# Kernel tuning notes

Hardware: AMD Instinct MI355X
Metric: run time of the kernel (lower is better)

## Reference

```python
import jax, jax.numpy as jnp
import numpy as np

DIM = 1024
N_HEADS = 16
HEAD_DIM = DIM // N_HEADS


def setup_inputs() -> dict:
    key = jax.random.key(0)
    ks = jax.random.split(key, 5)
    x = jax.random.normal(ks[0], (2, 2048, DIM), dtype=jnp.float32)
    # nn.Linear-style init scale
    s = 1.0 / np.sqrt(DIM)
    W_qkv = jax.random.uniform(ks[1], (DIM, 3 * DIM), jnp.float32, -s, s)
    b_qkv = jax.random.uniform(ks[2], (3 * DIM,), jnp.float32, -s, s)
    W_proj = jax.random.uniform(ks[3], (DIM, DIM), jnp.float32, -s, s)
    b_proj = jax.random.uniform(ks[4], (DIM,), jnp.float32, -s, s)
    return {"x": x, "W_qkv": W_qkv, "b_qkv": b_qkv, "W_proj": W_proj, "b_proj": b_proj}


def reference(x, W_qkv, b_qkv, W_proj, b_proj):
    B, S, D = x.shape
    scale = HEAD_DIM ** -0.5
    qkv = x @ W_qkv + b_qkv                                   # [B,S,3D]
    qkv = qkv.reshape(B, S, 3, N_HEADS, HEAD_DIM)
    q = qkv[:, :, 0].transpose(0, 2, 1, 3)                    # [B,H,S,d]
    k = qkv[:, :, 1].transpose(0, 2, 1, 3)
    v = qkv[:, :, 2].transpose(0, 2, 1, 3)
    attn = jnp.einsum('bhqd,bhkd->bhqk', q, k) * scale        # [B,H,S,S]
    attn = jax.nn.softmax(attn, axis=-1)
    out = jnp.einsum('bhqk,bhkd->bhqd', attn, v)              # [B,H,S,d]
    out = out.transpose(0, 2, 1, 3).reshape(B, S, D)
    return out @ W_proj + b_proj
```

## Files before the change

### kernel.cpp

```cpp
#include <hip/hip_runtime.h>
#include <stdint.h>

typedef unsigned short u16;
typedef __attribute__((ext_vector_type(8))) short bf16x8;
typedef __attribute__((ext_vector_type(4))) float f32x4;
typedef __attribute__((ext_vector_type(4))) u16 us4;
typedef __attribute__((ext_vector_type(8))) u16 us8;

__device__ __forceinline__ u16 f2bf(float f) {
  union { float f; unsigned u; } v; v.f = f;
  unsigned r = v.u + 0x7fffu + ((v.u >> 16) & 1u);
  return (u16)(r >> 16);
}

__device__ __forceinline__ void gld16(const void* g, void* l) {
  __builtin_amdgcn_global_load_lds(
      (const __attribute__((address_space(1))) void*)g,
      (__attribute__((address_space(3))) void*)l, 16, 0, 0);
}

__global__ void cvt_kernel(const float* __restrict__ in, u16* __restrict__ out, int n4) {
  int i = blockIdx.x * blockDim.x + threadIdx.x;
  if (i >= n4) return;
  f32x4 v = ((const f32x4*)in)[i];
  us4 r;
#pragma unroll
  for (int j = 0; j < 4; ++j) r[j] = f2bf(v[j]);
  ((us4*)out)[i] = r;
}

__global__ void transw_kernel(const float* __restrict__ in, u16* __restrict__ out, int R, int C) {
  __shared__ u16 tile[32][33];
  const int tx = threadIdx.x & 31, ty = threadIdx.x >> 5;
  const int c0 = blockIdx.x * 32, r0 = blockIdx.y * 32;
#pragma unroll
  for (int j = 0; j < 4; ++j)
    tile[ty + j * 8][tx] = f2bf(in[(size_t)(r0 + ty + j * 8) * C + c0 + tx]);
  __syncthreads();
#pragma unroll
  for (int j = 0; j < 4; ++j)
    out[(size_t)(c0 + ty + j * 8) * R + r0 + tx] = tile[tx][ty + j * 8];
}

__global__ __launch_bounds__(256) void qkv_gemm_kernel(
    const u16* __restrict__ A, const u16* __restrict__ Bt, const float* __restrict__ bias,
    u16* __restrict__ Qb, u16* __restrict__ Kb, u16* __restrict__ Vtb) {
  __shared__ u16 sm[17408];
  u16* As = sm;
  u16* Bs = sm + 4096;
  const int tid = threadIdx.x;
  const int w = tid >> 6, l = tid & 63, quad = l >> 4, lanelo = l & 15;
  const int wr = w >> 1, wc = w & 1;
  const long m0 = (long)blockIdx.x * 128;
  const long n0 = (long)blockIdx.y * 128;

  f32x4 acc[4][4];
#pragma unroll
  for (int i = 0; i < 4; ++i)
#pragma unroll
    for (int j = 0; j < 4; ++j) acc[i][j] = (f32x4){0.f, 0.f, 0.f, 0.f};

  const u16* ag = A + (m0 + w * 32 + (l >> 2)) * 1024 + (l & 3) * 8;
  const u16* bg = Bt + (n0 + w * 32 + (l >> 2)) * 1024 + (l & 3) * 8;
  u16* asl = As + w * 1024;
  u16* bsl = Bs + w * 1024;

  for (int kt = 0; kt < 32; ++kt) {
    const int ko = kt * 32;
    gld16(ag + ko, asl);
    gld16(ag + 16 * 1024 + ko, asl + 512);
    gld16(bg + ko, bsl);
    gld16(bg + 16 * 1024 + ko, bsl + 512);
    __syncthreads();
    bf16x8 af[4], bf[4];
#pragma unroll
    for (int mt = 0; mt < 4; ++mt)
      af[mt] = *(const bf16x8*)(As + (wr * 64 + mt * 16 + lanelo) * 32 + quad * 8);
#pragma unroll
    for (int nt = 0; nt < 4; ++nt)
      bf[nt] = *(const bf16x8*)(Bs + (wc * 64 + nt * 16 + lanelo) * 32 + quad * 8);
#pragma unroll
    for (int mt = 0; mt < 4; ++mt)
#pragma unroll
      for (int nt = 0; nt < 4; ++nt)
        acc[mt][nt] = __builtin_amdgcn_mfma_f32_16x16x32_bf16(af[mt], bf[nt], acc[mt][nt], 0, 0, 0);
    __syncthreads();
  }

  float bias_v[4];
#pragma unroll
  for (int nt = 0; nt < 4; ++nt) bias_v[nt] = bias[n0 + wc * 64 + nt * 16 + lanelo];

  u16* Ct = sm;
#pragma unroll
  for (int mt = 0; mt < 4; ++mt)
#pragma unroll
    for (int nt = 0; nt < 4; ++nt)
#pragma unroll
      for (int r = 0; r < 4; ++r)
        Ct[(wr * 64 + mt * 16 + quad * 4 + r) * 136 + wc * 64 + nt * 16 + lanelo] =
            f2bf(acc[mt][nt][r] + bias_v[nt]);
  __syncthreads();

  const int b = (int)(m0 >> 11);
  const int s0 = (int)(m0 & 2047);
  const int t = (int)(n0 >> 10);
  const int h0 = (int)((n0 & 1023) >> 6);

  if (t < 2) {
    u16* dst = (t == 0) ? Qb : Kb;
#pragma unroll
    for (int p = 0; p < 8; ++p) {
      const int hh = p >> 2;
      const int sl = (p & 3) * 32 + (tid >> 3);
      const int c8 = tid & 7;
      us8 v = *(const us8*)(Ct + sl * 136 + hh * 64 + c8 * 8);
      const int pos = (c8 + sl) & 7;
      const size_t off = ((size_t)((b * 16 + h0 + hh) * 2048 + s0 + sl)) * 64 + pos * 8;
      *(us8*)(dst + off) = v;
    }
  } else {
#pragma unroll
    for (int p = 0; p < 8; ++p) {
      const int hh = p >> 2;
      const int dl = (p & 3) * 16 + (tid >> 4);
      const int c16 = tid & 15;
      us8 v;
#pragma unroll
      for (int j = 0; j < 8; ++j) v[j] = Ct[(c16 * 8 + j) * 136 + hh * 64 + dl];
      const int pos = (c16 + dl) & 15;
      const size_t off = ((size_t)((b * 16 + h0 + hh) * 64 + dl)) * 2048 + s0 + pos * 8;
      *(us8*)(Vtb + off) = v;
    }
  }
}

__global__ __launch_bounds__(256) void attn_kernel(
    const u16* __restrict__ Qb, const u16* __restrict__ Kb,
    const u16* __restrict__ Vtb, u16* __restrict__ Ob) {
  __shared__ u16 Ks[128 * 64];
  __shared__ u16 Vs[64 * 128];
  __shared__ u16 Ps[4][32 * 128];
  const int tid = threadIdx.x;
  const int w = tid >> 6, l = tid & 63, quad = l >> 4, lanelo = l & 15;
  const int qt = blockIdx.x, head = blockIdx.y;
  const int b = head >> 4, h = head & 15;
  const u16* Qh = Qb + (size_t)head * 2048 * 64;
  const u16* Kh = Kb + (size_t)head * 2048 * 64;
  const u16* Vh = Vtb + (size_t)head * 64 * 2048;
  u16* Pw = &Ps[w][0];

  const float C = 0.18033688011112042f;

  bf16x8 qf[2][2];
#pragma unroll
  for (int mt = 0; mt < 2; ++mt)
#pragma unroll
    for (int ks = 0; ks < 2; ++ks) {
      const int row = qt * 128 + w * 32 + mt * 16 + lanelo;
      const int pos = (ks * 4 + quad + lanelo) & 7;
      qf[mt][ks] = *(const bf16x8*)(Qh + (size_t)row * 64 + pos * 8);
    }

  f32x4 o[2][4], os[2];
#pragma unroll
  for (int mt = 0; mt < 2; ++mt) {
    os[mt] = (f32x4){0.f, 0.f, 0.f, 0.f};
#pragma unroll
    for (int ot = 0; ot < 4; ++ot) o[mt][ot] = (f32x4){0.f, 0.f, 0.f, 0.f};
  }
  bf16x8 ones;
#pragma unroll
  for (int j = 0; j < 8; ++j) ones[j] = (short)0x3F80;

  for (int kt = 0; kt < 16; ++kt) {
    const u16* kbase = Kh + kt * 8192;
#pragma unroll
    for (int j = 0; j < 4; ++j) {
      const int i = w * 4 + j;
      gld16(kbase + i * 512 + l * 8, &Ks[i * 512]);
    }
#pragma unroll
    for (int j = 0; j < 4; ++j) {
      const int i = w * 4 + j;
      const int dd = i * 4 + (l >> 4);
      gld16(Vh + (size_t)dd * 2048 + kt * 128 + (l & 15) * 8, &Vs[i * 512]);
    }
    __syncthreads();

    f32x4 s[2][8];
#pragma unroll
    for (int mt = 0; mt < 2; ++mt)
#pragma unroll
      for (int nt = 0; nt < 8; ++nt) s[mt][nt] = (f32x4){0.f, 0.f, 0.f, 0.f};

#pragma unroll
    for (int ks = 0; ks < 2; ++ks) {
#pragma unroll
      for (int nt = 0; nt < 8; ++nt) {
        const int keyl = nt * 16 + lanelo;
        const int pos = (ks * 4 + quad + lanelo) & 7;
        bf16x8 kf = *(const bf16x8*)(&Ks[keyl * 64 + pos * 8]);
        s[0][nt] = __builtin_amdgcn_mfma_f32_16x16x32_bf16(qf[0][ks], kf, s[0][nt], 0, 0, 0);
        s[1][nt] = __builtin_amdgcn_mfma_f32_16x16x32_bf16(qf[1][ks], kf, s[1][nt], 0, 0, 0);
      }
    }

#pragma unroll
    for (int mt = 0; mt < 2; ++mt)
#pragma unroll
      for (int nt = 0; nt < 8; ++nt)
#pragma unroll
        for (int r = 0; r < 4; ++r) {
          const float p = exp2f(s[mt][nt][r] * C);
          const int row = mt * 16 + quad * 4 + r;
          const int pos = (2 * nt + (lanelo >> 3) + row) & 15;
          Pw[row * 128 + pos * 8 + (lanelo & 7)] = f2bf(p);
        }

#pragma unroll
    for (int ks = 0; ks < 4; ++ks) {
      bf16x8 pf[2];
#pragma unroll
      for (int mt = 0; mt < 2; ++mt) {
        const int row = mt * 16 + lanelo;
        const int pos = (ks * 4 + quad + lanelo) & 15;
        pf[mt] = *(const bf16x8*)(&Pw[row * 128 + pos * 8]);
      }
      os[0] = __builtin_amdgcn_mfma_f32_16x16x32_bf16(pf[0], ones, os[0], 0, 0, 0);
      os[1] = __builtin_amdgcn_mfma_f32_16x16x32_bf16(pf[1], ones, os[1], 0, 0, 0);
#pragma unroll
      for (int ot = 0; ot < 4; ++ot) {
        const int dim = ot * 16 + lanelo;
        const int pos = (ks * 4 + quad + lanelo) & 15;
        bf16x8 vf = *(const bf16x8*)(&Vs[dim * 128 + pos * 8]);
        o[0][ot] = __builtin_amdgcn_mfma_f32_16x16x32_bf16(pf[0], vf, o[0][ot], 0, 0, 0);
        o[1][ot] = __builtin_amdgcn_mfma_f32_16x16x32_bf16(pf[1], vf, o[1][ot], 0, 0, 0);
      }
    }
    __syncthreads();
  }

#pragma unroll
  for (int mt = 0; mt < 2; ++mt)
#pragma unroll
    for (int r = 0; r < 4; ++r) {
      const float inv = 1.0f / os[mt][r];
      const int srow = qt * 128 + w * 32 + mt * 16 + quad * 4 + r;
      const size_t base = ((size_t)(b * 2048 + srow)) * 1024 + h * 64;
#pragma unroll
      for (int ot = 0; ot < 4; ++ot)
        Ob[base + ot * 16 + lanelo] = f2bf(o[mt][ot][r] * inv);
    }
}

__global__ __launch_bounds__(256) void proj_gemm_kernel(
    const u16* __restrict__ A, const u16* __restrict__ Bt,
    const float* __restrict__ bias, float* __restrict__ out) {
  __shared__ u16 sm[8192];
  u16* As = sm;
  u16* Bs = sm + 4096;
  const int tid = threadIdx.x;
  const int w = tid >> 6, l = tid & 63, quad = l >> 4, lanelo = l & 15;
  const int wr = w >> 1, wc = w & 1;
  const long m0 = (long)blockIdx.x * 128;
  const long n0 = (long)blockIdx.y * 128;

  f32x4 acc[4][4];
#pragma unroll
  for (int i = 0; i < 4; ++i)
#pragma unroll
    for (int j = 0; j < 4; ++j) acc[i][j] = (f32x4){0.f, 0.f, 0.f, 0.f};

  const u16* ag = A + (m0 + w * 32 + (l >> 2)) * 1024 + (l & 3) * 8;
  const u16* bg = Bt + (n0 + w * 32 + (l >> 2)) * 1024 + (l & 3) * 8;
  u16* asl = As + w * 1024;
  u16* bsl = Bs + w * 1024;

  for (int kt = 0; kt < 32; ++kt) {
    const int ko = kt * 32;
    gld16(ag + ko, asl);
    gld16(ag + 16 * 1024 + ko, asl + 512);
    gld16(bg + ko, bsl);
    gld16(bg + 16 * 1024 + ko, bsl + 512);
    __syncthreads();
    bf16x8 af[4], bf[4];
#pragma unroll
    for (int mt = 0; mt < 4; ++mt)
      af[mt] = *(const bf16x8*)(As + (wr * 64 + mt * 16 + lanelo) * 32 + quad * 8);
#pragma unroll
    for (int nt = 0; nt < 4; ++nt)
      bf[nt] = *(const bf16x8*)(Bs + (wc * 64 + nt * 16 + lanelo) * 32 + quad * 8);
#pragma unroll
    for (int mt = 0; mt < 4; ++mt)
#pragma unroll
      for (int nt = 0; nt < 4; ++nt)
        acc[mt][nt] = __builtin_amdgcn_mfma_f32_16x16x32_bf16(af[mt], bf[nt], acc[mt][nt], 0, 0, 0);
    __syncthreads();
  }

  float bias_v[4];
#pragma unroll
  for (int nt = 0; nt < 4; ++nt) bias_v[nt] = bias[n0 + wc * 64 + nt * 16 + lanelo];

#pragma unroll
  for (int mt = 0; mt < 4; ++mt)
#pragma unroll
    for (int nt = 0; nt < 4; ++nt)
#pragma unroll
      for (int r = 0; r < 4; ++r) {
        const size_t m = m0 + wr * 64 + mt * 16 + quad * 4 + r;
        const size_t n = n0 + wc * 64 + nt * 16 + lanelo;
        out[m * 1024 + n] = acc[mt][nt][r] + bias_v[nt];
      }
}

extern "C" void kernel_launch(void* const* d_in, const int* in_sizes, int n_in,
                              void* d_out, int out_size, void* d_ws, size_t ws_size,
                              hipStream_t stream) {
  const float* x = (const float*)d_in[0];
  const float* Wqkv = (const float*)d_in[1];
  const float* bqkv = (const float*)d_in[2];
  const float* Wproj = (const float*)d_in[3];
  const float* bproj = (const float*)d_in[4];
  float* out = (float*)d_out;
  char* ws = (char*)d_ws;

  u16* Xb   = (u16*)(ws);
  u16* Ob   = (u16*)(ws);
  u16* Wqkt = (u16*)(ws + 8388608);
  u16* Wpt  = (u16*)(ws + 14680064);
  u16* Qb   = (u16*)(ws + 16777216);
  u16* Kb   = (u16*)(ws + 25165824);
  u16* Vtb  = (u16*)(ws + 33554432);

  cvt_kernel<<<4096, 256, 0, stream>>>(x, Xb, 1048576);
  transw_kernel<<<dim3(96, 32), 256, 0, stream>>>(Wqkv, Wqkt, 1024, 3072);
  transw_kernel<<<dim3(32, 32), 256, 0, stream>>>(Wproj, Wpt, 1024, 1024);
  qkv_gemm_kernel<<<dim3(32, 24), 256, 0, stream>>>(Xb, Wqkt, bqkv, Qb, Kb, Vtb);
  attn_kernel<<<dim3(16, 32), 256, 0, stream>>>(Qb, Kb, Vtb, Ob);
  proj_gemm_kernel<<<dim3(32, 8), 256, 0, stream>>>(Ob, Wpt, bproj, out);
}
```

Measured before the change: 218.0 us.

## Fold softmax scale into Q, transpose QK^T MFMA, pack P stores

The softmax scale (log2e/sqrt(d)) is applied to Q in the QKV GEMM epilogue, which removes a per-element multiply in the attention inner loop. Swapping the MFMA operands for S gives each lane four consecutive keys for one query row, so P can be written as packed 64-bit stores of two bf16 pairs. The exp uses the hardware exp2 builtin and a cheaper round-to-nearest-by-add bf16 pack. P is now processed in two halves, so the per-wave P buffer shrinks by half. The trade-offs are a slightly different bf16 rounding of P and Q being rounded after scaling.

```diff
diff --git a/kernel.cpp b/kernel.cpp
--- a/kernel.cpp
+++ b/kernel.cpp
@@ -11,6 +11,19 @@
   union { float f; unsigned u; } v; v.f = f;
   unsigned r = v.u + 0x7fffu + ((v.u >> 16) & 1u);
   return (u16)(r >> 16);
+}
+
+__device__ __forceinline__ unsigned pkbf(float a, float b) {
+  union { float f; unsigned u; } x, y; x.f = a; y.f = b;
+  return __builtin_amdgcn_perm(y.u + 0x8000u, x.u + 0x8000u, 0x07060302u);
+}
+
+__device__ __forceinline__ float fast_exp2(float x) {
+#if __has_builtin(__builtin_amdgcn_exp2f)
+  return __builtin_amdgcn_exp2f(x);
+#else
+  return exp2f(x);
+#endif
 }
 
 __device__ __forceinline__ void gld16(const void* g, void* l) {
@@ -87,6 +100,9 @@
     __syncthreads();
   }
 
+  const int t = (int)(n0 >> 10);
+  const float scl = (t == 0) ? 0.18033688011112042f : 1.0f;
+
   float bias_v[4];
 #pragma unroll
   for (int nt = 0; nt < 4; ++nt) bias_v[nt] = bias[n0 + wc * 64 + nt * 16 + lanelo];
@@ -99,12 +115,11 @@
 #pragma unroll
       for (int r = 0; r < 4; ++r)
         Ct[(wr * 64 + mt * 16 + quad * 4 + r) * 136 + wc * 64 + nt * 16 + lanelo] =
-            f2bf(acc[mt][nt][r] + bias_v[nt]);
+            f2bf((acc[mt][nt][r] + bias_v[nt]) * scl);
   __syncthreads();
 
   const int b = (int)(m0 >> 11);
   const int s0 = (int)(m0 & 2047);
-  const int t = (int)(n0 >> 10);
   const int h0 = (int)((n0 & 1023) >> 6);
 
   if (t < 2) {
@@ -140,7 +155,7 @@
     const u16* __restrict__ Vtb, u16* __restrict__ Ob) {
   __shared__ u16 Ks[128 * 64];
   __shared__ u16 Vs[64 * 128];
-  __shared__ u16 Ps[4][32 * 128];
+  __shared__ u16 Ps[4][32 * 64];
   const int tid = threadIdx.x;
   const int w = tid >> 6, l = tid & 63, quad = l >> 4, lanelo = l & 15;
   const int qt = blockIdx.x, head = blockIdx.y;
@@ -150,8 +165,6 @@
   const u16* Vh = Vtb + (size_t)head * 64 * 2048;
   u16* Pw = &Ps[w][0];
 
-  const float C = 0.18033688011112042f;
-
   bf16x8 qf[2][2];
 #pragma unroll
   for (int mt = 0; mt < 2; ++mt)
@@ -201,41 +214,49 @@
         const int keyl = nt * 16 + lanelo;
         const int pos = (ks * 4 + quad + lanelo) & 7;
         bf16x8 kf = *(const bf16x8*)(&Ks[keyl * 64 + pos * 8]);
-        s[0][nt] = __builtin_amdgcn_mfma_f32_16x16x32_bf16(qf[0][ks], kf, s[0][nt], 0, 0, 0);
-        s[1][nt] = __builtin_amdgcn_mfma_f32_16x16x32_bf16(qf[1][ks], kf, s[1][nt], 0, 0, 0);
+        s[0][nt] = __builtin_amdgcn_mfma_f32_16x16x32_bf16(kf, qf[0][ks], s[0][nt], 0, 0, 0);
+        s[1][nt] = __builtin_amdgcn_mfma_f32_16x16x32_bf16(kf, qf[1][ks], s[1][nt], 0, 0, 0);
       }
     }
 
 #pragma unroll
-    for (int mt = 0; mt < 2; ++mt)
-#pragma unroll
-      for (int nt = 0; nt < 8; ++nt)
-#pragma unroll
-        for (int r = 0; r < 4; ++r) {
-          const float p = exp2f(s[mt][nt][r] * C);
-          const int row = mt * 16 + quad * 4 + r;
-          const int pos = (2 * nt + (lanelo >> 3) + row) & 15;
-          Pw[row * 128 + pos * 8 + (lanelo & 7)] = f2bf(p);
+    for (int half = 0; half < 2; ++half) {
+#pragma unroll
+      for (int mt = 0; mt < 2; ++mt)
+#pragma unroll
+        for (int nt4 = 0; nt4 < 4; ++nt4) {
+          f32x4 sv = s[mt][half * 4 + nt4];
+          const float p0 = fast_exp2(sv[0]), p1 = fast_exp2(sv[1]);
+          const float p2 = fast_exp2(sv[2]), p3 = fast_exp2(sv[3]);
+          uint2 pk;
+          pk.x = pkbf(p0, p1);
+          pk.y = pkbf(p2, p3);
+          const int row = mt * 16 + lanelo;
+          const int chunk = nt4 * 2 + (quad >> 1);
+          const int pos = (chunk + lanelo) & 7;
+          *(uint2*)(&Pw[row * 64 + pos * 8 + (quad & 1) * 4]) = pk;
         }
 
 #pragma unroll
-    for (int ks = 0; ks < 4; ++ks) {
-      bf16x8 pf[2];
-#pragma unroll
-      for (int mt = 0; mt < 2; ++mt) {
-        const int row = mt * 16 + lanelo;
-        const int pos = (ks * 4 + quad + lanelo) & 15;
-        pf[mt] = *(const bf16x8*)(&Pw[row * 128 + pos * 8]);
-      }
-      os[0] = __builtin_amdgcn_mfma_f32_16x16x32_bf16(pf[0], ones, os[0], 0, 0, 0);
-      os[1] = __builtin_amdgcn_mfma_f32_16x16x32_bf16(pf[1], ones, os[1], 0, 0, 0);
-#pragma unroll
-      for (int ot = 0; ot < 4; ++ot) {
-        const int dim = ot * 16 + lanelo;
-        const int pos = (ks * 4 + quad + lanelo) & 15;
-        bf16x8 vf = *(const bf16x8*)(&Vs[dim * 128 + pos * 8]);
-        o[0][ot] = __builtin_amdgcn_mfma_f32_16x16x32_bf16(pf[0], vf, o[0][ot], 0, 0, 0);
-        o[1][ot] = __builtin_amdgcn_mfma_f32_16x16x32_bf16(pf[1], vf, o[1][ot], 0, 0, 0);
+      for (int ks2 = 0; ks2 < 2; ++ks2) {
+        bf16x8 pf[2];
+#pragma unroll
+        for (int mt = 0; mt < 2; ++mt) {
+          const int row = mt * 16 + lanelo;
+          const int pos = (ks2 * 4 + quad + lanelo) & 7;
+          pf[mt] = *(const bf16x8*)(&Pw[row * 64 + pos * 8]);
+        }
+        os[0] = __builtin_amdgcn_mfma_f32_16x16x32_bf16(pf[0], ones, os[0], 0, 0, 0);
+        os[1] = __builtin_amdgcn_mfma_f32_16x16x32_bf16(pf[1], ones, os[1], 0, 0, 0);
+        const int ksg = half * 2 + ks2;
+#pragma unroll
+        for (int ot = 0; ot < 4; ++ot) {
+          const int dim = ot * 16 + lanelo;
+          const int pos = (ksg * 4 + quad + lanelo) & 15;
+          bf16x8 vf = *(const bf16x8*)(&Vs[dim * 128 + pos * 8]);
+          o[0][ot] = __builtin_amdgcn_mfma_f32_16x16x32_bf16(pf[0], vf, o[0][ot], 0, 0, 0);
+          o[1][ot] = __builtin_amdgcn_mfma_f32_16x16x32_bf16(pf[1], vf, o[1][ot], 0, 0, 0);
+        }
       }
     }
     __syncthreads();
```

Result: faster. 195.0 us (-10.6%).
